# Performance work log

Measured on AMD Instinct MI355X. Metric: run time of the kernel, lower is better.

Reference implementation:

```python
import jax, jax.numpy as jnp
import numpy as np

B, S, D = 1, 2048, 1024
NH, NKV, WS = 8, 2, 64
HD = D // NH  # 128
E, HDIM, TOPK = 16, 512, 2
FP16_MIN = -65504.0
EPS = 1e-6
AUX_COEFF = 1e-5


def rmsnorm(x, w):
    return x * jax.lax.rsqrt(jnp.mean(x * x, axis=-1, keepdims=True) + EPS) * w


def setup_inputs() -> dict:
    key = jax.random.key(0)
    ks = jax.random.split(key, 24)
    r = lambda k, shape, fan: jax.random.normal(k, shape, dtype=jnp.float32) * (1.0 / np.sqrt(fan))
    return {
        "x": jax.random.normal(ks[0], (B, S, D), dtype=jnp.float32),
        "norm1_w": jnp.ones((D,), jnp.float32),
        "wq": r(ks[1], (D, NH * HD), D), "bq": jnp.zeros((NH * HD,), jnp.float32),
        "wk": r(ks[2], (D, NKV * HD), D), "bk": jnp.zeros((NKV * HD,), jnp.float32),
        "wv": r(ks[3], (D, NKV * HD), D), "bv": jnp.zeros((NKV * HD,), jnp.float32),
        "wo": r(ks[4], (NH * HD, D), NH * HD), "bo": jnp.zeros((D,), jnp.float32),
        "sink_bias": jnp.zeros((), jnp.float32),
        "norm2_w": jnp.ones((D,), jnp.float32),
        "router_w": r(ks[5], (D, E), D), "router_b": jnp.zeros((E,), jnp.float32),
        "w1": r(ks[6], (E, D, HDIM), D), "b1": jnp.zeros((E, HDIM), jnp.float32),
        "w2": r(ks[7], (E, HDIM, D), HDIM), "b2": jnp.zeros((E, D), jnp.float32),
    }


def reference(x, norm1_w, wq, bq, wk, bk, wv, bv, wo, bo, sink_bias,
              norm2_w, router_w, router_b, w1, b1, w2, b2):
    # ---- sliding-window attention with sink softmax ----
    h = rmsnorm(x, norm1_w)
    q = (h @ wq + bq).reshape(B, S, NH, HD).transpose(0, 2, 1, 3)    # [B,NH,S,HD]
    k = (h @ wk + bk).reshape(B, S, NKV, HD).transpose(0, 2, 1, 3)   # [B,NKV,S,HD]
    v = (h @ wv + bv).reshape(B, S, NKV, HD).transpose(0, 2, 1, 3)
    k = jnp.repeat(k, NH // NKV, axis=1)  # GQA expand -> [B,NH,S,HD]
    v = jnp.repeat(v, NH // NKV, axis=1)
    scores = jnp.einsum('bhqd,bhkd->bhqk', q, k) / np.sqrt(HD)
    i = jnp.arange(S)[:, None]
    j = jnp.arange(S)[None, :]
    band = (i - j >= 0) & (i - j <= WS - 1)  # causal sliding window
    scores = jnp.where(band, scores, FP16_MIN)
    m = jnp.maximum(jnp.max(scores, axis=-1, keepdims=True), sink_bias)
    ew = jnp.exp(scores - m)
    denom = jnp.sum(ew, axis=-1, keepdims=True) + jnp.exp(sink_bias - m)
    attn = ew / denom
    out = jnp.einsum('bhqk,bhkd->bhqd', attn, v).transpose(0, 2, 1, 3).reshape(B, S, D)
    x = x + (out @ wo + bo)

    # ---- MoE FFN ----
    h2 = rmsnorm(x, norm2_w)
    xf = h2.reshape(-1, D)                                  # [N,D]
    logits = (xf @ router_w + router_b) / 0.1               # [N,E]
    top_v, top_i = jax.lax.top_k(logits, TOPK)              # [N,k]
    top_w = jax.nn.softmax(top_v, axis=-1)
    probs = jax.nn.softmax(logits, axis=-1)
    aux_loss = jnp.sum(jnp.sum(probs, axis=0) ** 2) / E * AUX_COEFF
    # combine weights per (token, expert)
    gate = jnp.sum(jax.nn.one_hot(top_i, E, dtype=xf.dtype) * top_w[..., None], axis=1)  # [N,E]
    hmid = jax.nn.silu(jnp.einsum('nd,edh->neh', xf, w1) + b1)   # [N,E,H]
    y = jnp.einsum('neh,ehd->ned', hmid, w2) + b2                # [N,E,D]
    ffn = jnp.einsum('ne,ned->nd', gate, y)
    x = x + ffn.reshape(B, S, D)
    return x, aux_loss
```

## Files before the change

### kernel.cpp

```cpp
#include <hip/hip_runtime.h>
#include <hip/hip_bf16.h>

#define S     2048
#define D     1024
#define NH    8
#define NKV   2
#define HD    128
#define WS_   64
#define E_    16
#define HDIM  512
#define TOPK  2
#define NTOK  S
#define NSLOT (S*TOPK)
#define QKV_M (D + 2*NKV*HD)
#define KOFF  D
#define VOFF  (D + NKV*HD)
#define QB    8
#define WROWS (QB + WS_ - 1)
#define KPITCH 73
#define VPADF  132

typedef __attribute__((ext_vector_type(8))) short bf16x8;
typedef __attribute__((ext_vector_type(4))) float floatx4;

__device__ inline short f2bf(float f) {
    __hip_bfloat16 b = __float2bfloat16(f);
    return *reinterpret_cast<short*>(&b);
}

__global__ __launch_bounds__(256) void tconv_all(
    const float* __restrict__ wq, const float* __restrict__ wk,
    const float* __restrict__ wv, const float* __restrict__ wo,
    const float* __restrict__ w1, const float* __restrict__ w2,
    const float* __restrict__ bq, const float* __restrict__ bk,
    const float* __restrict__ bv, const float* __restrict__ router_w,
    short* __restrict__ wqkvT, short* __restrict__ woT,
    short* __restrict__ w1T, short* __restrict__ w2T,
    float* __restrict__ bqkv, float* __restrict__ rwT)
{
    int id = blockIdx.x;
    if (id >= 18950) {
        int ky = id - 18950;
        int t = threadIdx.x;
        int r = t >> 4, c = t & 15;
        int k0 = ky * 32;
        rwT[c * D + k0 + r]      = router_w[(k0 + r) * E_ + c];
        rwT[c * D + k0 + r + 16] = router_w[(k0 + r + 16) * E_ + c];
        return;
    }
    if (id >= 18944) {
        int t = (id - 18944) * 256 + threadIdx.x;
        if (t < D) bqkv[t] = bq[t];
        else if (t < VOFF) bqkv[t] = bk[t - D];
        else bqkv[t] = bv[t - VOFF];
        return;
    }
    const float* in; short* outp; int K, M, mx, ky;
    if (id < 1024)      { in = wq; outp = wqkvT;                  K = D; M = D;   int l = id;        mx = l & 31; ky = l >> 5; }
    else if (id < 1280) { in = wk; outp = wqkvT + (size_t)KOFF*D; K = D; M = 256; int l = id - 1024; mx = l & 7;  ky = l >> 3; }
    else if (id < 1536) { in = wv; outp = wqkvT + (size_t)VOFF*D; K = D; M = 256; int l = id - 1280; mx = l & 7;  ky = l >> 3; }
    else if (id < 2560) { in = wo; outp = woT;                    K = D; M = D;   int l = id - 1536; mx = l & 31; ky = l >> 5; }
    else if (id < 10752){ int l = id - 2560;  int e = l >> 9; int r = l & 511;
                          in = w1 + (size_t)e * D * HDIM; outp = w1T + (size_t)e * D * HDIM;
                          K = D; M = HDIM; mx = r & 15; ky = r >> 4; }
    else                { int l = id - 10752; int e = l >> 9; int r = l & 511;
                          in = w2 + (size_t)e * D * HDIM; outp = w2T + (size_t)e * D * HDIM;
                          K = HDIM; M = D; mx = r & 31; ky = r >> 5; }
    __shared__ float tile[32][33];
    int t = threadIdx.x, r = t >> 3, c4 = (t & 7) * 4;
    int k0 = ky * 32, m0 = mx * 32;
    float4 v = *(const float4*)&in[(size_t)(k0 + r) * M + m0 + c4];
    tile[r][c4 + 0] = v.x; tile[r][c4 + 1] = v.y;
    tile[r][c4 + 2] = v.z; tile[r][c4 + 3] = v.w;
    __syncthreads();
    short4 o;
    o.x = f2bf(tile[c4 + 0][r]);
    o.y = f2bf(tile[c4 + 1][r]);
    o.z = f2bf(tile[c4 + 2][r]);
    o.w = f2bf(tile[c4 + 3][r]);
    *(short4*)&outp[(size_t)(m0 + r) * K + k0 + c4] = o;
}

__global__ __launch_bounds__(256) void rmsnorm_kernel(
    const float* __restrict__ x, const float* __restrict__ w,
    short* __restrict__ outb)
{
    int row = blockIdx.x, t = threadIdx.x;
    float4 v = ((const float4*)(x + (size_t)row * D))[t];
    float ss = v.x*v.x + v.y*v.y + v.z*v.z + v.w*v.w;
    #pragma unroll
    for (int off = 32; off; off >>= 1) ss += __shfl_xor(ss, off, 64);
    __shared__ float red[4];
    if ((t & 63) == 0) red[t >> 6] = ss;
    __syncthreads();
    float total = red[0] + red[1] + red[2] + red[3];
    float scale = rsqrtf(total * (1.0f / (float)D) + 1e-6f);
    float4 wv = ((const float4*)w)[t];
    short4 ob;
    ob.x = f2bf(v.x * scale * wv.x); ob.y = f2bf(v.y * scale * wv.y);
    ob.z = f2bf(v.z * scale * wv.z); ob.w = f2bf(v.w * scale * wv.w);
    ((short4*)(outb + (size_t)row * D))[t] = ob;
}

template <int V>
__global__ __launch_bounds__(256) void mgemm(
    const short* __restrict__ A, const short* __restrict__ Bt,
    const float* __restrict__ bias, float* __restrict__ C,
    short* __restrict__ Cb, const float* __restrict__ res, int K, int M,
    const int* __restrict__ offs, const float* __restrict__ tok_gate)
{
    int e = (V >= 2) ? blockIdx.z : 0;
    const short* Bte = (V >= 2) ? Bt + (size_t)e * M * K : Bt;
    const float* be  = (V >= 2) ? bias + (size_t)e * M : bias;

    int row_lo, row_hi;
    if (V >= 2) {
        row_lo = offs[e] + blockIdx.y * 64;
        row_hi = offs[e + 1];
        if (row_lo >= row_hi) return;
    } else {
        row_lo = blockIdx.y * 64;
        row_hi = 1 << 30;
    }
    int col0 = blockIdx.x * 64;

    constexpr int SUB = 64 * 40;
    constexpr int BUF = 2 * SUB;
    __shared__ short As[2 * BUF];
    __shared__ short Bs[2 * BUF];

    int t = threadIdx.x;
    int srow = t >> 2;
    int skq  = t & 3;
    int sgk  = skq * 16;
    int ssub = skq >> 1;
    int soff = (skq & 1) * 16;

    int  agrow = row_lo + srow;
    bool aval  = (V < 2) || (agrow < row_hi);
    int  asrc  = aval ? agrow : row_lo;
    const short* aptr = A   + (size_t)asrc * K + sgk;
    const short* bptr = Bte + (size_t)(col0 + srow) * K + sgk;
    short* as_w = &As[ssub * SUB + srow * 40 + soff];
    short* bs_w = &Bs[ssub * SUB + srow * 40 + soff];

    int lane = t & 63, wave = t >> 6;
    int wm = (wave & 1) * 32, wn = (wave >> 1) * 32;
    int rin = lane & 15, quad = lane >> 4;

    floatx4 acc[2][2];
    #pragma unroll
    for (int i = 0; i < 2; ++i)
        #pragma unroll
        for (int j = 0; j < 2; ++j)
            acc[i][j] = (floatx4){0.f, 0.f, 0.f, 0.f};

    float4 va0 = *(const float4*)(aptr);
    float4 va1 = *(const float4*)(aptr + 8);
    float4 vb0 = *(const float4*)(bptr);
    float4 vb1 = *(const float4*)(bptr + 8);
    *(float4*)(as_w)     = va0;
    *(float4*)(as_w + 8) = va1;
    *(float4*)(bs_w)     = vb0;
    *(float4*)(bs_w + 8) = vb1;
    if (K > 64) {
        va0 = *(const float4*)(aptr + 64);
        va1 = *(const float4*)(aptr + 72);
        vb0 = *(const float4*)(bptr + 64);
        vb1 = *(const float4*)(bptr + 72);
    }
    __syncthreads();

    const int NIT = K >> 6;
    for (int it = 0; it < NIT; ++it) {
        int cur = it & 1, nxt = cur ^ 1;
        if (it + 1 < NIT) {
            *(float4*)(as_w + nxt * BUF)     = va0;
            *(float4*)(as_w + nxt * BUF + 8) = va1;
            *(float4*)(bs_w + nxt * BUF)     = vb0;
            *(float4*)(bs_w + nxt * BUF + 8) = vb1;
            if (it + 2 < NIT) {
                int k2 = (it + 2) << 6;
                va0 = *(const float4*)(aptr + k2);
                va1 = *(const float4*)(aptr + k2 + 8);
                vb0 = *(const float4*)(bptr + k2);
                vb1 = *(const float4*)(bptr + k2 + 8);
            }
        }
        #pragma unroll
        for (int s = 0; s < 2; ++s) {
            bf16x8 af[2], bfr[2];
            #pragma unroll
            for (int i = 0; i < 2; ++i)
                af[i] = *(const bf16x8*)&As[cur * BUF + s * SUB
                                            + (wm + i * 16 + rin) * 40 + quad * 8];
            #pragma unroll
            for (int j = 0; j < 2; ++j)
                bfr[j] = *(const bf16x8*)&Bs[cur * BUF + s * SUB
                                             + (wn + j * 16 + rin) * 40 + quad * 8];
            #pragma unroll
            for (int i = 0; i < 2; ++i)
                #pragma unroll
                for (int j = 0; j < 2; ++j)
                    acc[i][j] = __builtin_amdgcn_mfma_f32_16x16x32_bf16(
                        af[i], bfr[j], acc[i][j], 0, 0, 0);
        }
        __syncthreads();
    }

    #pragma unroll
    for (int i = 0; i < 2; ++i) {
        #pragma unroll
        for (int j = 0; j < 2; ++j) {
            int cg = col0 + wn + j * 16 + rin;
            #pragma unroll
            for (int rr = 0; rr < 4; ++rr) {
                int rg = row_lo + wm + i * 16 + quad * 4 + rr;
                float val = acc[i][j][rr];
                if (V == 0) {
                    C[(size_t)rg * M + cg] = val + be[cg];
                } else if (V == 1) {
                    C[(size_t)rg * M + cg] = val + be[cg] + res[(size_t)rg * M + cg];
                } else if (V == 2) {
                    if (rg < row_hi) {
                        float vb_ = val + be[cg];
                        Cb[(size_t)rg * M + cg] = f2bf(vb_ / (1.f + __expf(-vb_)));
                    }
                } else {
                    if (rg < row_hi)
                        C[(size_t)rg * M + cg] = tok_gate[rg] * (val + be[cg]);
                }
            }
        }
    }
}

__global__ __launch_bounds__(256) void attn_kernel(
    const float* __restrict__ qkv, const float* __restrict__ sink_ptr,
    short* __restrict__ ao)
{
    __shared__ __align__(16) float KT[32 * KPITCH * 4];
    __shared__ __align__(16) float Vs[WROWS * VPADF];
    __shared__ __align__(16) float Ps4[4][64][4];

    int qblk = blockIdx.x;
    int kvh  = blockIdx.y;
    int q0   = qblk * QB;
    int jbase = q0 - (WS_ - 1);

    int t = threadIdx.x;
    int c4 = (t & 31) * 4, c4g = t & 31;
    for (int r = t >> 5; r < WROWS; r += 8) {
        int j = jbase + r;
        float4 kv4 = make_float4(0.f, 0.f, 0.f, 0.f);
        float4 vv4 = make_float4(0.f, 0.f, 0.f, 0.f);
        if (j >= 0) {
            kv4 = *(const float4*)(qkv + (size_t)j * QKV_M + KOFF + kvh * HD + c4);
            vv4 = *(const float4*)(qkv + (size_t)j * QKV_M + VOFF + kvh * HD + c4);
        }
        *(float4*)&KT[(c4g * KPITCH + r) * 4] = kv4;
        *(float4*)&Vs[r * VPADF + c4] = vv4;
    }
    __syncthreads();

    int lane = t & 63, wv = t >> 6;
    float sink = sink_ptr[0];
    const float rscale = 0.08838834764831845f;

    #pragma unroll
    for (int g = 0; g < 2; ++g) {
        int qi = wv * 2 + g;
        int i  = q0 + qi;
        bool valid = (jbase + qi + lane) >= 0;

        float sc[4] = {0.f, 0.f, 0.f, 0.f};
        const float* qbase = qkv + (size_t)i * QKV_M + (kvh * 4) * HD;
        #pragma unroll
        for (int c = 0; c < 32; ++c) {
            float4 kx = *(const float4*)&KT[(c * KPITCH + qi + lane) * 4];
            #pragma unroll
            for (int hh = 0; hh < 4; ++hh) {
                float4 q4 = *(const float4*)(qbase + hh * HD + c * 4);
                sc[hh] += q4.x*kx.x + q4.y*kx.y + q4.z*kx.z + q4.w*kx.w;
            }
        }

        float pn[4];
        #pragma unroll
        for (int hh = 0; hh < 4; ++hh) {
            float s = valid ? sc[hh] * rscale : -1e30f;
            float m = s;
            #pragma unroll
            for (int off = 32; off; off >>= 1) m = fmaxf(m, __shfl_xor(m, off, 64));
            float mf = fmaxf(m, sink);
            float p  = __expf(s - mf);
            float ds = p;
            #pragma unroll
            for (int off = 32; off; off >>= 1) ds += __shfl_xor(ds, off, 64);
            pn[hh] = p / (ds + __expf(sink - mf));
        }
        *(float4*)&Ps4[wv][lane][0] = make_float4(pn[0], pn[1], pn[2], pn[3]);

        float o0=0,o1=0,o2=0,o3=0,o4=0,o5=0,o6=0,o7=0;
        const float* vp = &Vs[qi * VPADF + 2 * lane];
        #pragma unroll
        for (int jj = 0; jj < 64; ++jj) {
            float4 p4 = *(const float4*)&Ps4[wv][jj][0];
            float2 vv = *(const float2*)(vp + jj * VPADF);
            o0 += p4.x * vv.x; o1 += p4.x * vv.y;
            o2 += p4.y * vv.x; o3 += p4.y * vv.y;
            o4 += p4.z * vv.x; o5 += p4.z * vv.y;
            o6 += p4.w * vv.x; o7 += p4.w * vv.y;
        }
        short2 r0; r0.x = f2bf(o0); r0.y = f2bf(o1);
        short2 r1; r1.x = f2bf(o2); r1.y = f2bf(o3);
        short2 r2; r2.x = f2bf(o4); r2.y = f2bf(o5);
        short2 r3; r3.x = f2bf(o6); r3.y = f2bf(o7);
        ((short2*)(ao + (size_t)i * D + (kvh * 4 + 0) * HD))[lane] = r0;
        ((short2*)(ao + (size_t)i * D + (kvh * 4 + 1) * HD))[lane] = r1;
        ((short2*)(ao + (size_t)i * D + (kvh * 4 + 2) * HD))[lane] = r2;
        ((short2*)(ao + (size_t)i * D + (kvh * 4 + 3) * HD))[lane] = r3;
    }
}

__global__ __launch_bounds__(256) void rms_router_kernel(
    const float* __restrict__ x1, const float* __restrict__ w,
    short* __restrict__ h2b, const float* __restrict__ rwT,
    const float* __restrict__ rb, float* __restrict__ probs,
    int* __restrict__ top_i, float* __restrict__ top_g)
{
    int tok = blockIdx.x, t = threadIdx.x;
    __shared__ float hrow[D];
    float4 v = ((const float4*)(x1 + (size_t)tok * D))[t];
    float ss = v.x*v.x + v.y*v.y + v.z*v.z + v.w*v.w;
    #pragma unroll
    for (int off = 32; off; off >>= 1) ss += __shfl_xor(ss, off, 64);
    __shared__ float red[4];
    if ((t & 63) == 0) red[t >> 6] = ss;
    __syncthreads();
    float total = red[0] + red[1] + red[2] + red[3];
    float scale = rsqrtf(total * (1.0f / (float)D) + 1e-6f);
    float4 wv = ((const float4*)w)[t];
    float4 o;
    o.x = v.x * scale * wv.x; o.y = v.y * scale * wv.y;
    o.z = v.z * scale * wv.z; o.w = v.w * scale * wv.w;
    ((float4*)hrow)[t] = o;
    short4 ob;
    ob.x = f2bf(o.x); ob.y = f2bf(o.y); ob.z = f2bf(o.z); ob.w = f2bf(o.w);
    ((short4*)(h2b + (size_t)tok * D))[t] = ob;
    __syncthreads();

    int e = t & 15, seg = t >> 4;
    const float4* rwp = (const float4*)(rwT + (size_t)e * D + seg * 64);
    const float4* hp  = (const float4*)(hrow + seg * 64);
    float part = 0.f;
    #pragma unroll
    for (int i = 0; i < 16; ++i) {
        float4 a = hp[i];
        float4 b = rwp[i];
        part += a.x * b.x; part += a.y * b.y;
        part += a.z * b.z; part += a.w * b.w;
    }
    __shared__ float lpart[256];
    lpart[t] = part;
    __syncthreads();
    __shared__ float logits[E_];
    if (t < E_) {
        float sl = 0.f;
        for (int sg = 0; sg < 16; ++sg) sl += lpart[sg * 16 + t];
        logits[t] = (sl + rb[t]) * 10.0f;
    }
    __syncthreads();
    __shared__ float sm[2];
    if (t == 0) {
        float mx = logits[0];
        for (int x = 1; x < E_; ++x) mx = fmaxf(mx, logits[x]);
        float ps = 0.f;
        for (int x = 0; x < E_; ++x) ps += __expf(logits[x] - mx);
        sm[0] = mx; sm[1] = ps;
        int i0 = 0; float v0 = logits[0];
        for (int x = 1; x < E_; ++x) if (logits[x] > v0) { v0 = logits[x]; i0 = x; }
        int i1 = (i0 == 0) ? 1 : 0; float v1 = logits[i1];
        for (int x = 0; x < E_; ++x) {
            if (x == i0) continue;
            if (logits[x] > v1) { v1 = logits[x]; i1 = x; }
        }
        float e1 = __expf(v1 - v0);
        float g0 = 1.f / (1.f + e1);
        float g1 = e1 * g0;
        top_i[tok * 2 + 0] = i0; top_g[tok * 2 + 0] = g0;
        top_i[tok * 2 + 1] = i1; top_g[tok * 2 + 1] = g1;
    }
    __syncthreads();
    if (t < E_) probs[tok * E_ + t] = __expf(logits[t] - sm[0]) / sm[1];
}

__global__ __launch_bounds__(256) void finalize_kernel(
    const float* __restrict__ probs, const int* __restrict__ top_i,
    int* __restrict__ offs, int* __restrict__ cursor,
    float* __restrict__ aux_out)
{
    __shared__ float csum[E_];
    __shared__ int hist[E_];
    int t = threadIdx.x;
    if (t < E_) { csum[t] = 0.f; hist[t] = 0; }
    __syncthreads();

    int c = t & 15, g = t >> 4;
    float part = 0.f;
    for (int i = 0; i < NTOK / 16; ++i)
        part += probs[(size_t)(i * 16 + g) * E_ + c];
    atomicAdd(&csum[c], part);

    for (int i = 0; i < NSLOT / 256; ++i) {
        int eidx = top_i[i * 256 + t] & 15;
        atomicAdd(&hist[eidx], 1);
    }
    __syncthreads();

    if (t == 0) {
        int acc = 0;
        for (int e = 0; e < E_; ++e) { offs[e] = acc; cursor[e] = acc; acc += hist[e]; }
        offs[E_] = acc;
        float s = 0.f;
        for (int e = 0; e < E_; ++e) s += csum[e] * csum[e];
        *aux_out = s / (float)E_ * 1e-5f;
    }
}

__global__ __launch_bounds__(256) void scatter_kernel(
    const int* __restrict__ top_i, const float* __restrict__ top_g,
    int* __restrict__ cursor, int* __restrict__ tok_idx,
    float* __restrict__ tok_gate, int* __restrict__ slot_of)
{
    int tok = blockIdx.x * 256 + threadIdx.x;
    if (tok >= NTOK) return;
    for (int s = 0; s < TOPK; ++s) {
        int e = top_i[tok * 2 + s] & 15;
        int pos = atomicAdd(&cursor[e], 1) & (NSLOT - 1);
        tok_idx[pos]  = tok;
        tok_gate[pos] = top_g[tok * 2 + s];
        slot_of[tok * 2 + s] = pos;
    }
}

__global__ __launch_bounds__(256) void gather_kernel(
    const short* __restrict__ h2b, const int* __restrict__ tok_idx,
    short* __restrict__ xg)
{
    int slot = blockIdx.x * 2 + (threadIdx.x >> 7);
    int c = (threadIdx.x & 127) * 8;
    int tok = tok_idx[slot] & (NTOK - 1);
    *(float4*)&xg[(size_t)slot * D + c] =
        *(const float4*)&h2b[(size_t)tok * D + c];
}

__global__ __launch_bounds__(256) void combine_kernel(
    const float* __restrict__ x1, const float* __restrict__ y,
    const int* __restrict__ slot_of, float* __restrict__ out)
{
    int tok = blockIdx.x, t = threadIdx.x;
    int s0 = slot_of[tok * 2] & (NSLOT - 1), s1 = slot_of[tok * 2 + 1] & (NSLOT - 1);
    float4 a = ((const float4*)(x1 + (size_t)tok * D))[t];
    float4 b = ((const float4*)(y + (size_t)s0 * D))[t];
    float4 c = ((const float4*)(y + (size_t)s1 * D))[t];
    float4 o;
    o.x = a.x + b.x + c.x; o.y = a.y + b.y + c.y;
    o.z = a.z + b.z + c.z; o.w = a.w + b.w + c.w;
    ((float4*)(out + (size_t)tok * D))[t] = o;
}

extern "C" void kernel_launch(void* const* d_in, const int* in_sizes, int n_in,
                              void* d_out, int out_size, void* d_ws, size_t ws_size,
                              hipStream_t stream)
{
    const float* x        = (const float*)d_in[0];
    const float* norm1_w  = (const float*)d_in[1];
    const float* wq       = (const float*)d_in[2];
    const float* bq       = (const float*)d_in[3];
    const float* wk       = (const float*)d_in[4];
    const float* bk       = (const float*)d_in[5];
    const float* wv       = (const float*)d_in[6];
    const float* bv       = (const float*)d_in[7];
    const float* wo       = (const float*)d_in[8];
    const float* bo       = (const float*)d_in[9];
    const float* sink     = (const float*)d_in[10];
    const float* norm2_w  = (const float*)d_in[11];
    const float* router_w = (const float*)d_in[12];
    const float* router_b = (const float*)d_in[13];
    const float* w1       = (const float*)d_in[14];
    const float* b1       = (const float*)d_in[15];
    const float* w2       = (const float*)d_in[16];
    const float* b2       = (const float*)d_in[17];
    float* out = (float*)d_out;

    char* w = (char*)d_ws;
    auto alloc = [&](size_t bytes) {
        char* p = w; w += (bytes + 255) & ~255ull; return p;
    };
    short* wqkvT = (short*)alloc((size_t)QKV_M * D * 2);
    short* woT   = (short*)alloc((size_t)D * D * 2);
    short* w1T   = (short*)alloc((size_t)E_ * HDIM * D * 2);
    short* w2T   = (short*)alloc((size_t)E_ * D * HDIM * 2);
    float* bqkv  = (float*)alloc(QKV_M * 4);
    float* rwT   = (float*)alloc((size_t)E_ * D * 4);
    short* h_bf  = (short*)alloc((size_t)S * D * 2);
    float* qkv   = (float*)alloc((size_t)S * QKV_M * 4);
    float* x1    = (float*)alloc((size_t)S * D * 4);
    short* h2b   = (short*)alloc((size_t)S * D * 2);
    short* xg    = (short*)alloc((size_t)NSLOT * D * 2);
    float* yslot = (float*)alloc((size_t)NSLOT * D * 4);
    float* probs = (float*)alloc((size_t)NTOK * E_ * 4);
    int*   offs     = (int*)alloc(17 * 4);
    int*   cursor   = (int*)alloc(16 * 4);
    int*   top_i    = (int*)alloc((size_t)NSLOT * 4);
    float* top_g    = (float*)alloc((size_t)NSLOT * 4);
    int*   tok_idx  = (int*)alloc((size_t)NSLOT * 4);
    float* tok_gate = (float*)alloc((size_t)NSLOT * 4);
    int*   slot_of  = (int*)alloc((size_t)NSLOT * 4);
    short* ao_bf = h_bf;
    short* hmid  = (short*)qkv;

    tconv_all<<<18982, 256, 0, stream>>>(wq, wk, wv, wo, w1, w2, bq, bk, bv,
                                         router_w, wqkvT, woT, w1T, w2T,
                                         bqkv, rwT);

    rmsnorm_kernel<<<S, 256, 0, stream>>>(x, norm1_w, h_bf);

    mgemm<0><<<dim3(QKV_M / 64, S / 64), 256, 0, stream>>>(
        h_bf, wqkvT, bqkv, qkv, nullptr, nullptr, D, QKV_M, nullptr, nullptr);

    attn_kernel<<<dim3(S / QB, NKV), 256, 0, stream>>>(qkv, sink, ao_bf);

    mgemm<1><<<dim3(D / 64, S / 64), 256, 0, stream>>>(
        ao_bf, woT, bo, x1, nullptr, x, D, D, nullptr, nullptr);

    rms_router_kernel<<<NTOK, 256, 0, stream>>>(x1, norm2_w, h2b, rwT,
                                                router_b, probs, top_i, top_g);

    finalize_kernel<<<1, 256, 0, stream>>>(probs, top_i, offs, cursor,
                                           out + (size_t)S * D);

    scatter_kernel<<<(NTOK + 255) / 256, 256, 0, stream>>>(
        top_i, top_g, cursor, tok_idx, tok_gate, slot_of);

    gather_kernel<<<NSLOT / 2, 256, 0, stream>>>(h2b, tok_idx, xg);

    mgemm<2><<<dim3(HDIM / 64, NSLOT / 64, E_), 256, 0, stream>>>(
        xg, w1T, b1, nullptr, hmid, nullptr, D, HDIM, offs, nullptr);

    mgemm<3><<<dim3(D / 64, NSLOT / 64, E_), 256, 0, stream>>>(
        hmid, w2T, b2, yslot, nullptr, nullptr, HDIM, D, offs, tok_gate);

    combine_kernel<<<NTOK, 256, 0, stream>>>(x1, yslot, slot_of, out);
}
```

Before: 298.8 us.

## Enlarge GEMM tiles to 128x128 with direct global-to-LDS loads and XOR swizzle

Rewrites the shared bf16 MFMA GEMM to use 128x128 output tiles, with each wave computing a 64x64 sub-tile of 4x4 MFMA accumulators. Operand tiles are now fetched with global_load_lds straight into an XOR-swizzled LDS layout instead of being staged through registers into a padded layout. The aim is more data reuse per tile and fewer register round trips for loads. In exchange it raises register and LDS use and launches far fewer blocks, which hurts occupancy and load balance, especially for the small per-expert MoE GEMMs. The async LDS writes also need waitcnt/barrier ordering to be correct.

Result: slower. 324.7 us (+8.7%).

```diff
diff --git a/kernel.cpp b/kernel.cpp
--- a/kernel.cpp
+++ b/kernel.cpp
@@ -102,6 +102,16 @@
     ((short4*)(outb + (size_t)row * D))[t] = ob;
 }
 
+#define BT   128
+#define BKS  64
+#define BUFS (BT * BKS)
+
+__device__ inline void gld16(const short* g, short* l) {
+    __builtin_amdgcn_global_load_lds(
+        (const __attribute__((address_space(1))) unsigned int*)g,
+        (__attribute__((address_space(3))) unsigned int*)l, 16, 0, 0);
+}
+
 template <int V>
 __global__ __launch_bounds__(256) void mgemm(
     const short* __restrict__ A, const short* __restrict__ Bt,
@@ -115,93 +125,84 @@
 
     int row_lo, row_hi;
     if (V >= 2) {
-        row_lo = offs[e] + blockIdx.y * 64;
+        row_lo = offs[e] + blockIdx.y * BT;
         row_hi = offs[e + 1];
         if (row_lo >= row_hi) return;
     } else {
-        row_lo = blockIdx.y * 64;
+        row_lo = blockIdx.y * BT;
         row_hi = 1 << 30;
     }
-    int col0 = blockIdx.x * 64;
-
-    constexpr int SUB = 64 * 40;
-    constexpr int BUF = 2 * SUB;
-    __shared__ short As[2 * BUF];
-    __shared__ short Bs[2 * BUF];
+    int col0 = blockIdx.x * BT;
+
+    __shared__ __align__(16) short As[2 * BUFS];
+    __shared__ __align__(16) short Bs[2 * BUFS];
 
     int t = threadIdx.x;
-    int srow = t >> 2;
-    int skq  = t & 3;
-    int sgk  = skq * 16;
-    int ssub = skq >> 1;
-    int soff = (skq & 1) * 16;
-
-    int  agrow = row_lo + srow;
-    bool aval  = (V < 2) || (agrow < row_hi);
-    int  asrc  = aval ? agrow : row_lo;
-    const short* aptr = A   + (size_t)asrc * K + sgk;
-    const short* bptr = Bte + (size_t)(col0 + srow) * K + sgk;
-    short* as_w = &As[ssub * SUB + srow * 40 + soff];
-    short* bs_w = &Bs[ssub * SUB + srow * 40 + soff];
-
-    int lane = t & 63, wave = t >> 6;
-    int wm = (wave & 1) * 32, wn = (wave >> 1) * 32;
+    int wave = t >> 6, lane = t & 63;
+    int lrow   = lane >> 3;
+    int schunk = (lane & 7) ^ lrow;
+
+    const short* aQ[4];
+    const short* bQ[4];
+    #pragma unroll
+    for (int c = 0; c < 4; ++c) {
+        int row = (wave * 4 + c) * 8 + lrow;
+        int gr = row_lo + row;
+        if (V >= 2 && gr >= row_hi) gr = row_lo;
+        aQ[c] = A   + (size_t)gr * K + (schunk << 3);
+        bQ[c] = Bte + (size_t)(col0 + row) * K + (schunk << 3);
+    }
+
     int rin = lane & 15, quad = lane >> 4;
-
-    floatx4 acc[2][2];
-    #pragma unroll
-    for (int i = 0; i < 2; ++i)
+    int wm = (wave & 1) * 64, wn = (wave >> 1) * 64;
+
+    floatx4 acc[4][4];
+    #pragma unroll
+    for (int i = 0; i < 4; ++i)
         #pragma unroll
-        for (int j = 0; j < 2; ++j)
+        for (int j = 0; j < 4; ++j)
             acc[i][j] = (floatx4){0.f, 0.f, 0.f, 0.f};
 
-    float4 va0 = *(const float4*)(aptr);
-    float4 va1 = *(const float4*)(aptr + 8);
-    float4 vb0 = *(const float4*)(bptr);
-    float4 vb1 = *(const float4*)(bptr + 8);
-    *(float4*)(as_w)     = va0;
-    *(float4*)(as_w + 8) = va1;
-    *(float4*)(bs_w)     = vb0;
-    *(float4*)(bs_w + 8) = vb1;
-    if (K > 64) {
-        va0 = *(const float4*)(aptr + 64);
-        va1 = *(const float4*)(aptr + 72);
-        vb0 = *(const float4*)(bptr + 64);
-        vb1 = *(const float4*)(bptr + 72);
-    }
-    __syncthreads();
-
     const int NIT = K >> 6;
+
+    #pragma unroll
+    for (int c = 0; c < 4; ++c) gld16(aQ[c], &As[(wave * 4 + c) * 512]);
+    #pragma unroll
+    for (int c = 0; c < 4; ++c) gld16(bQ[c], &Bs[(wave * 4 + c) * 512]);
+    __syncthreads();
+
     for (int it = 0; it < NIT; ++it) {
         int cur = it & 1, nxt = cur ^ 1;
         if (it + 1 < NIT) {
-            *(float4*)(as_w + nxt * BUF)     = va0;
-            *(float4*)(as_w + nxt * BUF + 8) = va1;
-            *(float4*)(bs_w + nxt * BUF)     = vb0;
-            *(float4*)(bs_w + nxt * BUF + 8) = vb1;
-            if (it + 2 < NIT) {
-                int k2 = (it + 2) << 6;
-                va0 = *(const float4*)(aptr + k2);
-                va1 = *(const float4*)(aptr + k2 + 8);
-                vb0 = *(const float4*)(bptr + k2);
-                vb1 = *(const float4*)(bptr + k2 + 8);
-            }
-        }
+            int kk = (it + 1) << 6;
+            #pragma unroll
+            for (int c = 0; c < 4; ++c)
+                gld16(aQ[c] + kk, &As[nxt * BUFS + (wave * 4 + c) * 512]);
+            #pragma unroll
+            for (int c = 0; c < 4; ++c)
+                gld16(bQ[c] + kk, &Bs[nxt * BUFS + (wave * 4 + c) * 512]);
+        }
+        const short* Ab = &As[cur * BUFS];
+        const short* Bb = &Bs[cur * BUFS];
         #pragma unroll
         for (int s = 0; s < 2; ++s) {
-            bf16x8 af[2], bfr[2];
-            #pragma unroll
-            for (int i = 0; i < 2; ++i)
-                af[i] = *(const bf16x8*)&As[cur * BUF + s * SUB
-                                            + (wm + i * 16 + rin) * 40 + quad * 8];
-            #pragma unroll
-            for (int j = 0; j < 2; ++j)
-                bfr[j] = *(const bf16x8*)&Bs[cur * BUF + s * SUB
-                                             + (wn + j * 16 + rin) * 40 + quad * 8];
-            #pragma unroll
-            for (int i = 0; i < 2; ++i)
+            bf16x8 af[4], bfr[4];
+            #pragma unroll
+            for (int i = 0; i < 4; ++i) {
+                int row = wm + i * 16 + rin;
+                af[i] = *(const bf16x8*)&Ab[row * BKS
+                        + ((((s << 2) | quad) ^ (rin & 7)) << 3)];
+            }
+            #pragma unroll
+            for (int j = 0; j < 4; ++j) {
+                int row = wn + j * 16 + rin;
+                bfr[j] = *(const bf16x8*)&Bb[row * BKS
+                        + ((((s << 2) | quad) ^ (rin & 7)) << 3)];
+            }
+            #pragma unroll
+            for (int i = 0; i < 4; ++i)
                 #pragma unroll
-                for (int j = 0; j < 2; ++j)
+                for (int j = 0; j < 4; ++j)
                     acc[i][j] = __builtin_amdgcn_mfma_f32_16x16x32_bf16(
                         af[i], bfr[j], acc[i][j], 0, 0, 0);
         }
@@ -209,9 +210,9 @@
     }
 
     #pragma unroll
-    for (int i = 0; i < 2; ++i) {
+    for (int i = 0; i < 4; ++i) {
         #pragma unroll
-        for (int j = 0; j < 2; ++j) {
+        for (int j = 0; j < 4; ++j) {
             int cg = col0 + wn + j * 16 + rin;
             #pragma unroll
             for (int rr = 0; rr < 4; ++rr) {
@@ -527,12 +528,12 @@
 
     rmsnorm_kernel<<<S, 256, 0, stream>>>(x, norm1_w, h_bf);
 
-    mgemm<0><<<dim3(QKV_M / 64, S / 64), 256, 0, stream>>>(
+    mgemm<0><<<dim3(QKV_M / BT, S / BT), 256, 0, stream>>>(
         h_bf, wqkvT, bqkv, qkv, nullptr, nullptr, D, QKV_M, nullptr, nullptr);
 
     attn_kernel<<<dim3(S / QB, NKV), 256, 0, stream>>>(qkv, sink, ao_bf);
 
-    mgemm<1><<<dim3(D / 64, S / 64), 256, 0, stream>>>(
+    mgemm<1><<<dim3(D / BT, S / BT), 256, 0, stream>>>(
         ao_bf, woT, bo, x1, nullptr, x, D, D, nullptr, nullptr);
 
     rms_router_kernel<<<NTOK, 256, 0, stream>>>(x1, norm2_w, h2b, rwT,
@@ -546,10 +547,10 @@
 
     gather_kernel<<<NSLOT / 2, 256, 0, stream>>>(h2b, tok_idx, xg);
 
-    mgemm<2><<<dim3(HDIM / 64, NSLOT / 64, E_), 256, 0, stream>>>(
+    mgemm<2><<<dim3(HDIM / BT, NSLOT / BT, E_), 256, 0, stream>>>(
         xg, w1T, b1, nullptr, hmid, nullptr, D, HDIM, offs, nullptr);
 
-    mgemm<3><<<dim3(D / 64, NSLOT / 64, E_), 256, 0, stream>>>(
+    mgemm<3><<<dim3(D / BT, NSLOT / BT, E_), 256, 0, stream>>>(
         hmid, w2T, b2, yslot, nullptr, nullptr, HDIM, D, offs, tok_gate);
 
     combine_kernel<<<NTOK, 256, 0, stream>>>(x1, yslot, slot_of, out);
```
